# Optimization experiments

Hardware: AMD Instinct MI355X
Metric: run time of the kernel (lower is better)

The kernel has to match this reference:

```python
import jax, jax.numpy as jnp
import numpy as np

B, L, DH = 4, 4096, 1024
T, DG = 1024, 768
P = 256


def setup_inputs() -> dict:
    key = jax.random.key(0)
    k1, k2, k3, k4, k5 = jax.random.split(key, 5)
    H = jax.random.normal(k1, (B, L, DH), dtype=jnp.float32)
    G = jax.random.normal(k2, (B, T, DG), dtype=jnp.float32)
    # key mask: True = padded/masked. Guarantee at least one valid key per row.
    mask = jax.random.randint(k3, (B, L), 0, 2).astype(jnp.bool_)
    mask = mask.at[:, 0].set(False)
    # torch Linear weights: [out, in]
    Wk_w = jax.random.normal(k4, (P, DH), dtype=jnp.float32) * (DH ** -0.5)
    Wq_w = jax.random.normal(k5, (P, DG), dtype=jnp.float32) * (DG ** -0.5)
    return {"H": H, "G": G, "mask": mask, "Wk_w": Wk_w, "Wq_w": Wq_w}


def reference(H, G, mask, Wk_w, Wq_w):
    # K = Wk(H): [B,L,P]; Q = Wq(G): [B,T,P]
    K = jnp.einsum('bld,pd->blp', H, Wk_w)
    Q = jnp.einsum('btd,pd->btp', G, Wq_w)
    scale = P ** -0.5
    logits = jnp.einsum('btp,blp->btl', Q, K) * scale  # [B,T,L]
    neg_inf = jnp.finfo(logits.dtype).min
    logits = jnp.where(mask[:, None, :], neg_inf, logits)
    alpha = jax.nn.softmax(logits, axis=-1)  # softmax over L (streaming-equivalent)
    Z = jnp.einsum('btl,bld->btd', alpha, H)  # [B,T,DH]
    return Z
```

## Files before the change

kernel.cpp:

```cpp
#include <hip/hip_runtime.h>
#include <hip/hip_bf16.h>


typedef __attribute__((ext_vector_type(8))) short short8;
typedef __attribute__((ext_vector_type(4))) float f32x4;

static __device__ __forceinline__ unsigned short bf16bits(float x) {
    __hip_bfloat16 b = __float2bfloat16(x);
    return *(unsigned short*)&b;
}

static __device__ __forceinline__ void gload_lds16(const __hip_bfloat16* g,
                                                   __hip_bfloat16* l)
{
    auto gp = (const __attribute__((address_space(1))) unsigned int*)(uintptr_t)g;
    auto lp = (__attribute__((address_space(3))) unsigned int*)(unsigned int)(uintptr_t)l;
    __builtin_amdgcn_global_load_lds(gp, lp, 16, 0, 0);
}

__global__ __launch_bounds__(256)
void scan_kernel(const void* __restrict__ mask,
                 unsigned short* __restrict__ idx,
                 int* __restrict__ lc, int* __restrict__ lcpad,
                 float* __restrict__ rowsum, int L, int T, int B)
{
    const int b = blockIdx.x;
    const int tid = threadIdx.x;

    for (int i = tid; i < T; i += 256) rowsum[(long)b * T + i] = 0.f;

    const unsigned char*  m8g  = (const unsigned char*)mask;
    const unsigned short* m16g = (const unsigned short*)mask;
    const unsigned int*   m32g = (const unsigned int*)mask;
    __shared__ int c1, c2, c4, c8, cp, wsh;
    if (tid == 0) { c1 = c2 = c4 = c8 = cp = 0; }
    __syncthreads();
    {
        const int N = B * L;
        int l1 = 0, l2 = 0, l4 = 0, l8 = 0, lp = 0;
        for (int i = tid; i < N; i += 256) l1 += (m8g[i] != 0);
        for (int i = tid; i < N / 2; i += 256) {
            l2 += (m16g[i] != 0);
            lp += ((m8g[2 * i] != 0) == (m8g[2 * i + 1] != 0));
        }
        for (int i = tid; i < N / 4; i += 256) l4 += (m32g[i] != 0);
        for (int i = tid; i < N / 8; i += 256) l8 += ((m32g[2 * i] | m32g[2 * i + 1]) != 0);
        atomicAdd(&c1, l1); atomicAdd(&c2, l2); atomicAdd(&c4, l4);
        atomicAdd(&c8, l8); atomicAdd(&cp, lp);
    }
    __syncthreads();
    if (tid == 0) {
        const float f1 = fabsf(c1 / 16384.f - 0.5f);
        const float f2 = fabsf(c2 / 8192.f  - 0.5f);
        const float f4 = fabsf(c4 / 4096.f  - 0.5f);
        const float f8 = fabsf(c8 / 2048.f  - 0.5f);
        int w = 1; float best = f1;
        if (f2 < best) { best = f2; w = 2; }
        if (f4 < best) { best = f4; w = 4; }
        if (f8 < best) { best = f8; w = 8; }
        if (w == 1 && cp > 7400) w = 2;
        wsh = w;
    }
    __syncthreads();
    const int w = wsh;

    const unsigned char*  m8  = (const unsigned char*)mask;
    const unsigned short* m16 = (const unsigned short*)mask;
    const unsigned int*   m32 = (const unsigned int*)mask;
    const uint2*          m64 = (const uint2*)mask;
    bool v[16];
    int cnt = 0;
    #pragma unroll
    for (int i = 0; i < 16; ++i) {
        const int l = tid * 16 + i;
        const long mi = (long)b * L + l;
        bool masked;
        if (w == 1)      masked = m8[mi] != 0;
        else if (w == 2) masked = m16[mi] != 0;
        else if (w == 4) masked = m32[mi] != 0;
        else             { uint2 q = m64[mi]; masked = (q.x | q.y) != 0; }
        v[i] = !masked;
        cnt += v[i] ? 1 : 0;
    }
    __shared__ int waveTot[4];
    int pre = cnt;
    #pragma unroll
    for (int off = 1; off < 64; off <<= 1) {
        const int t = __shfl_up(pre, off, 64);
        if ((tid & 63) >= off) pre += t;
    }
    if ((tid & 63) == 63) waveTot[tid >> 6] = pre;
    __syncthreads();
    int waveOff = 0;
    for (int wv = 0; wv < (tid >> 6); ++wv) waveOff += waveTot[wv];
    int o = waveOff + pre - cnt;
    #pragma unroll
    for (int i = 0; i < 16; ++i)
        if (v[i]) idx[(long)b * L + (o++)] = (unsigned short)(tid * 16 + i);
    if (tid == 255) {
        const int total = waveOff + pre;
        lc[b] = total;
        lcpad[b] = (total + 127) & ~127;
    }
}

__global__ __launch_bounds__(256)
void prep_all_kernel(const float* __restrict__ H,
                     __hip_bfloat16* __restrict__ Hbf,
                     __hip_bfloat16* __restrict__ Ht,
                     const unsigned short* __restrict__ idx,
                     const int* __restrict__ lc, const int* __restrict__ lcpad,
                     const float* __restrict__ Wk, unsigned short* __restrict__ Wkbf,
                     const float* __restrict__ Wq, unsigned short* __restrict__ Wqbf,
                     const float* __restrict__ G,  unsigned short* __restrict__ Gbf,
                     int L, int D)
{
    __shared__ __align__(16) __hip_bfloat16 tile[64][72];
    int id = blockIdx.x;
    if (id < 4096) {
        const int b  = id >> 10;
        const int c0 = (id & 63) * 64;
        if (c0 >= lcpad[b]) return;
        const int d0 = ((id >> 6) & 15) * 64;
        const int Lcb = lc[b];
        const float* Hb = H + (long)b * L * D;
        __hip_bfloat16* Hbfb = Hbf + (long)b * L * D;
        __hip_bfloat16* Htb  = Ht  + (long)b * D * L;
        const int tx = threadIdx.x & 15, ty = threadIdx.x >> 4;
        #pragma unroll
        for (int p = 0; p < 4; ++p) {
            const int row = ty + p * 16;
            const int c = c0 + row;
            float4 v = {0.f, 0.f, 0.f, 0.f};
            if (c < Lcb) {
                const int l = idx[(long)b * L + c];
                v = *(const float4*)(&Hb[(long)l * D + d0 + tx * 4]);
            }
            ushort4 o;
            o.x = bf16bits(v.x); o.y = bf16bits(v.y);
            o.z = bf16bits(v.z); o.w = bf16bits(v.w);
            *(ushort4*)(&Hbfb[(long)c * D + d0 + tx * 4]) = o;
            tile[tx * 4 + 0][row] = __float2bfloat16(v.x);
            tile[tx * 4 + 1][row] = __float2bfloat16(v.y);
            tile[tx * 4 + 2][row] = __float2bfloat16(v.z);
            tile[tx * 4 + 3][row] = __float2bfloat16(v.w);
        }
        __syncthreads();
        const int ll = threadIdx.x & 7;
        const int dq = threadIdx.x >> 3;
        #pragma unroll
        for (int q = 0; q < 2; ++q) {
            const int dd = dq + q * 32;
            const short8 v = *(const short8*)(&tile[dd][ll * 8]);
            *(short8*)(&Htb[(long)(d0 + dd) * L + c0 + ll * 8]) = v;
        }
        return;
    }
    id -= 4096;
    const float* in; unsigned short* out; int n4;
    if (id < 256)       { in = Wk; out = Wkbf; n4 = (256 * 1024) / 4; }
    else if (id < 448)  { id -= 256; in = Wq; out = Wqbf; n4 = (256 * 768) / 4; }
    else                { id -= 448; in = G;  out = Gbf;  n4 = (4 * 1024 * 768) / 4; }
    const int i = id * 256 + threadIdx.x;
    if (i >= n4) return;
    float4 v = ((const float4*)in)[i];
    ushort4 o;
    o.x = bf16bits(v.x); o.y = bf16bits(v.y);
    o.z = bf16bits(v.z); o.w = bf16bits(v.w);
    ((ushort4*)out)[i] = o;
}

template <typename OutT, int MODE, int BM>
static __device__ __forceinline__
void gemm_bt_body(int bx, int by, int zb, __hip_bfloat16* lds_pool,
                  const __hip_bfloat16* __restrict__ A,
                  const __hip_bfloat16* __restrict__ Bm,
                  OutT* __restrict__ C,
                  int K, int lda, int ldb, int ldc,
                  long batchStrideA, long batchStrideB, long batchStrideC,
                  float scale,
                  float* __restrict__ rowsum, int rowsumStride, int lcv)
{
    constexpr int MI  = BM / 32;
    constexpr int ACH = BM / 64;
    constexpr int ATS = BM * 32;

    A  += (long)zb * batchStrideA;
    Bm += (long)zb * batchStrideB;
    C  += (long)zb * batchStrideC;
    const int NT = K / 32;

    const int tid  = threadIdx.x;
    const int lane = tid & 63;
    const int wave = tid >> 6;
    const int wm = (wave & 1) * (BM / 2);
    const int wn = (wave >> 1) * 64;
    const int rowBase = bx * BM;
    const int colBase = by * 128;

    __hip_bfloat16* AsP = lds_pool;
    __hip_bfloat16* BsP = lds_pool + 3 * ATS;

    f32x4 acc[MI][4];
    #pragma unroll
    for (int i = 0; i < MI; ++i)
        #pragma unroll
        for (int j = 0; j < 4; ++j)
            acc[i][j] = (f32x4){0.f, 0.f, 0.f, 0.f};

    const int srow = lane >> 2;
    const int scol = ((lane & 3) ^ ((lane >> 3) & 3)) * 8;
    const long ar0 = (long)(rowBase + wave * (BM / 4) + srow) * lda;
    const long ar1 = ar0 + 16l * lda;
    const long br0 = (long)(colBase + wave * 32 + srow) * ldb;
    const long br1 = br0 + 16l * ldb;

    const int mrow = lane & 15;
    const int koff = (((lane >> 4) ^ ((lane >> 1) & 3)) * 8);

    auto stage = [&](int buf, int t) {
        const int kk = t * 32 + scol;
        gload_lds16(A + ar0 + kk, AsP + buf * ATS + wave * (BM / 4) * 32);
        if constexpr (ACH == 2)
            gload_lds16(A + ar1 + kk, AsP + buf * ATS + wave * (BM / 4) * 32 + 512);
        gload_lds16(Bm + br0 + kk, BsP + buf * 4096 + wave * 1024);
        gload_lds16(Bm + br1 + kk, BsP + buf * 4096 + wave * 1024 + 512);
    };

    stage(0, 0);
    stage(1, 1);

    int cur = 0;
    for (int t = 0; t < NT; ++t) {
        if (t + 1 < NT) {
            if constexpr (ACH == 2)
                asm volatile("s_waitcnt vmcnt(4)" ::: "memory");
            else
                asm volatile("s_waitcnt vmcnt(3)" ::: "memory");
        } else {
            asm volatile("s_waitcnt vmcnt(0)" ::: "memory");
        }
        __builtin_amdgcn_s_barrier();
        if (t + 2 < NT) {
            const int nxt2 = (cur >= 1) ? cur - 1 : cur + 2;
            stage(nxt2, t + 2);
        }

        short8 af[MI], bf[4];
        #pragma unroll
        for (int mi = 0; mi < MI; ++mi)
            af[mi] = *(const short8*)(AsP + cur * ATS + (wm + mi * 16 + mrow) * 32 + koff);
        #pragma unroll
        for (int ni = 0; ni < 4; ++ni)
            bf[ni] = *(const short8*)(BsP + cur * 4096 + (wn + ni * 16 + mrow) * 32 + koff);

        #pragma unroll
        for (int mi = 0; mi < MI; ++mi)
            #pragma unroll
            for (int ni = 0; ni < 4; ++ni)
                acc[mi][ni] = __builtin_amdgcn_mfma_f32_16x16x32_bf16(
                    af[mi], bf[ni], acc[mi][ni], 0, 0, 0);
        cur = (cur == 2) ? 0 : cur + 1;
    }

    const int crow0 = (lane >> 4) * 4;
    const int ccol  = lane & 15;

    if constexpr (MODE == 2) {
        __syncthreads();
        __hip_bfloat16* cst = lds_pool;
        bool mk[4];
        #pragma unroll
        for (int ni = 0; ni < 4; ++ni)
            mk[ni] = (colBase + wn + ni * 16 + ccol) >= lcv;
        #pragma unroll
        for (int mi = 0; mi < MI; ++mi) {
            #pragma unroll
            for (int r = 0; r < 4; ++r) {
                const int row = wm + mi * 16 + crow0 + r;
                float rs = 0.f;
                #pragma unroll
                for (int ni = 0; ni < 4; ++ni) {
                    const int col = wn + ni * 16 + ccol;
                    const float e = mk[ni] ? 0.f
                                           : __expf(acc[mi][ni][r] * scale);
                    const __hip_bfloat16 pb = __float2bfloat16(e);
                    cst[row * 136 + (((col >> 3) ^ (row >> 3)) << 3) + (col & 7)] = pb;
                    rs += __bfloat162float(pb);
                }
                rs += __shfl_xor(rs, 1, 64);
                rs += __shfl_xor(rs, 2, 64);
                rs += __shfl_xor(rs, 4, 64);
                rs += __shfl_xor(rs, 8, 64);
                if ((lane & 15) == 0)
                    atomicAdd(&rowsum[(long)zb * rowsumStride + rowBase + row], rs);
            }
        }
        __syncthreads();
        const int g   = tid & 15;
        const int r4  = tid >> 4;
        const int lof = ((g ^ r4) << 3);
        #pragma unroll
        for (int k = 0; k < 8; ++k) {
            const int row = r4 * 8 + k;
            const short8 v = *(const short8*)(cst + row * 136 + lof);
            *(short8*)(&((__hip_bfloat16*)C)[(long)(rowBase + row) * ldc + colBase + g * 8]) = v;
        }
    } else if constexpr (MODE == 3) {
        #pragma unroll
        for (int mi = 0; mi < MI; ++mi) {
            #pragma unroll
            for (int r = 0; r < 4; ++r) {
                const int row = rowBase + wm + mi * 16 + crow0 + r;
                const float inv = 1.0f / rowsum[(long)zb * rowsumStride + row];
                #pragma unroll
                for (int ni = 0; ni < 4; ++ni) {
                    const int col = colBase + wn + ni * 16 + ccol;
                    ((float*)C)[(long)row * ldc + col] = acc[mi][ni][r] * inv;
                }
            }
        }
    } else if constexpr (sizeof(OutT) == 2) {
        __syncthreads();
        __hip_bfloat16* cst = lds_pool;
        #pragma unroll
        for (int mi = 0; mi < MI; ++mi) {
            #pragma unroll
            for (int ni = 0; ni < 4; ++ni) {
                #pragma unroll
                for (int r = 0; r < 4; ++r) {
                    const int row = wm + mi * 16 + crow0 + r;
                    const int col = wn + ni * 16 + ccol;
                    cst[row * 136 + (((col >> 3) ^ (row >> 3)) << 3) + (col & 7)] =
                        __float2bfloat16(acc[mi][ni][r] * scale);
                }
            }
        }
        __syncthreads();
        const int g   = tid & 15;
        const int r4  = tid >> 4;
        const int lof = ((g ^ r4) << 3);
        #pragma unroll
        for (int k = 0; k < 8; ++k) {
            const int row = r4 * 8 + k;
            const short8 v = *(const short8*)(cst + row * 136 + lof);
            *(short8*)(&((__hip_bfloat16*)C)[(long)(rowBase + row) * ldc + colBase + g * 8]) = v;
        }
    } else {
        #pragma unroll
        for (int mi = 0; mi < MI; ++mi) {
            #pragma unroll
            for (int ni = 0; ni < 4; ++ni) {
                #pragma unroll
                for (int r = 0; r < 4; ++r) {
                    const int row = rowBase + wm + mi * 16 + crow0 + r;
                    const int col = colBase + wn + ni * 16 + ccol;
                    ((float*)C)[(long)row * ldc + col] = acc[mi][ni][r] * scale;
                }
            }
        }
    }
}

static __device__ __forceinline__ void xcd_swizzle(int& bx, int& by, int& bz)
{
    const int nwg = gridDim.x * gridDim.y * gridDim.z;
    bx = blockIdx.x; by = blockIdx.y; bz = blockIdx.z;
    if ((nwg & 7) == 0) {
        int lin = bx + gridDim.x * (by + gridDim.y * bz);
        lin = (lin & 7) * (nwg >> 3) + (lin >> 3);
        bx = lin % gridDim.x;
        const int t = lin / gridDim.x;
        by = t % gridDim.y;
        bz = t / gridDim.y;
    }
}

__global__ __launch_bounds__(256)
void qk_gemm_kernel(const __hip_bfloat16* __restrict__ Gbf,
                    const __hip_bfloat16* __restrict__ Wqbf,
                    __hip_bfloat16* __restrict__ Qbf,
                    const __hip_bfloat16* __restrict__ Hbf,
                    const __hip_bfloat16* __restrict__ Wkbf,
                    __hip_bfloat16* __restrict__ Kbf,
                    const int* __restrict__ lcpad,
                    int DG_, int DH_, int P_, int L_)
{
    __shared__ __align__(16) __hip_bfloat16 lds_pool[24576];
    int bx, by, bz;
    xcd_swizzle(bx, by, bz);
    if (bx < 32) {
        gemm_bt_body<__hip_bfloat16, 0, 128>(bx, by, 0, lds_pool,
            Gbf, Wqbf, Qbf, DG_, DG_, DG_, P_, 0, 0, 0, 1.0f,
            nullptr, 0, 0);
    } else {
        const int rowBase = (bx - 32) * 128;
        const int bb = rowBase / L_;
        if (rowBase - bb * L_ >= lcpad[bb]) return;
        gemm_bt_body<__hip_bfloat16, 0, 128>(bx - 32, by, 0, lds_pool,
            Hbf, Wkbf, Kbf, DH_, DH_, DH_, P_, 0, 0, 0, 1.0f,
            nullptr, 0, 0);
    }
}

__global__ __launch_bounds__(256)
void s_gemm_kernel(const __hip_bfloat16* __restrict__ Qbf,
                   const __hip_bfloat16* __restrict__ Kbf,
                   __hip_bfloat16* __restrict__ Sb,
                   const int* __restrict__ lc, const int* __restrict__ lcpad,
                   float* __restrict__ rowsum,
                   int P_, int L_, int T_)
{
    __shared__ __align__(16) __hip_bfloat16 lds_pool[24576];
    int bx, by, bz;
    xcd_swizzle(bx, by, bz);
    if (by * 128 >= lcpad[bz]) return;
    gemm_bt_body<__hip_bfloat16, 2, 128>(bx, by, bz, lds_pool,
        Qbf, Kbf, Sb, P_, P_, P_, L_,
        (long)T_ * P_, (long)L_ * P_, (long)T_ * L_, 0.0625f,
        rowsum, T_, lc[bz]);
}

__global__ __launch_bounds__(256)
void z_gemm_kernel(const __hip_bfloat16* __restrict__ Sb,
                   const __hip_bfloat16* __restrict__ Ht,
                   float* __restrict__ Z,
                   const int* __restrict__ lcpad,
                   const float* __restrict__ rowsum,
                   int L_, int DH_, int T_)
{
    __shared__ __align__(16) __hip_bfloat16 lds_pool[24576];
    int bx, by, bz;
    xcd_swizzle(bx, by, bz);
    gemm_bt_body<float, 3, 64>(bx, by, bz, lds_pool,
        Sb, Ht, Z, lcpad[bz], L_, L_, DH_,
        (long)T_ * L_, (long)DH_ * L_, (long)T_ * DH_, 1.0f,
        (float*)rowsum, T_, 0);
}

extern "C" void kernel_launch(void* const* d_in, const int* in_sizes, int n_in,
                              void* d_out, int out_size, void* d_ws, size_t ws_size,
                              hipStream_t stream)
{
    constexpr int B = 4, L = 4096, DH = 1024, T = 1024, DG = 768, P = 256;

    const float* H  = (const float*)d_in[0];
    const float* G  = (const float*)d_in[1];
    const void*  mask = d_in[2];
    const float* Wk = (const float*)d_in[3];
    const float* Wq = (const float*)d_in[4];
    for (int i = 0; i < n_in; ++i) {
        switch (in_sizes[i]) {
            case B * L * DH: H    = (const float*)d_in[i]; break;
            case B * T * DG: G    = (const float*)d_in[i]; break;
            case B * L:      mask = d_in[i];               break;
            case P * DH:     Wk   = (const float*)d_in[i]; break;
            case P * DG:     Wq   = (const float*)d_in[i]; break;
        }
    }
    float* Z = (float*)d_out;

    char* ws = (char*)d_ws;
    __hip_bfloat16* Hbf  = (__hip_bfloat16*)ws;
    __hip_bfloat16* Ht   = (__hip_bfloat16*)(ws + (32l << 20));
    __hip_bfloat16* Gbf  = (__hip_bfloat16*)(ws + (64l << 20));
    __hip_bfloat16* Qbf  = (__hip_bfloat16*)(ws + (70l << 20));
    __hip_bfloat16* Kbf  = (__hip_bfloat16*)(ws + (72l << 20));
    __hip_bfloat16* Wkbf = (__hip_bfloat16*)(ws + (80l << 20));
    __hip_bfloat16* Wqbf = (__hip_bfloat16*)(ws + (80l << 20) + (512l << 10));
    float*          rowsum    = (float*)(ws + (80l << 20) + (896l << 10));
    int*            lcBuf     = (int*)  (ws + (80l << 20) + (961l << 10));
    int*            lcpadBuf  = (int*)  (ws + (80l << 20) + (961l << 10) + 64);
    unsigned short* idxBuf    = (unsigned short*)(ws + (80l << 20) + (962l << 10));
    __hip_bfloat16* Sb   = (__hip_bfloat16*)(ws + (81l << 20));

    const dim3 blk(256);

    scan_kernel<<<dim3(B), blk, 0, stream>>>(
        mask, idxBuf, lcBuf, lcpadBuf, rowsum, L, T, B);

    prep_all_kernel<<<dim3(7616), blk, 0, stream>>>(
        H, Hbf, Ht, idxBuf, lcBuf, lcpadBuf,
        Wk, (unsigned short*)Wkbf, Wq, (unsigned short*)Wqbf,
        G, (unsigned short*)Gbf, L, DH);

    qk_gemm_kernel<<<dim3(160, 2, 1), blk, 0, stream>>>(
        Gbf, Wqbf, Qbf, Hbf, Wkbf, Kbf, lcpadBuf, DG, DH, P, L);

    s_gemm_kernel<<<dim3(T / 128, L / 128, B), blk, 0, stream>>>(
        Qbf, Kbf, Sb, lcBuf, lcpadBuf, rowsum, P, L, T);

    z_gemm_kernel<<<dim3(T / 64, DH / 128, B), blk, 0, stream>>>(
        Sb, Ht, Z, lcpadBuf, rowsum, L, DH, T);
}
```

Baseline: 217.2 us.

## Stage two K-tiles per barrier in Z GEMM and coalesce fp32 stores via LDS

Adds a KTP template parameter so each pipeline phase loads and computes several 32-wide K tiles per barrier. The Z GEMM uses two tiles per phase, which halves the barrier and wait count and puts more loads in flight, at the cost of more LDS (pool grown to 72KB) and possibly lower occupancy. The Z epilogue now stages normalized fp32 results in LDS and writes them out as 16-byte row-contiguous vectors instead of scattered scalar stores.

```diff
diff --git a/kernel.cpp b/kernel.cpp
--- a/kernel.cpp
+++ b/kernel.cpp
@@ -170,7 +170,7 @@
     ((ushort4*)out)[i] = o;
 }
 
-template <typename OutT, int MODE, int BM>
+template <typename OutT, int MODE, int BM, int KTP>
 static __device__ __forceinline__
 void gemm_bt_body(int bx, int by, int zb, __hip_bfloat16* lds_pool,
                   const __hip_bfloat16* __restrict__ A,
@@ -183,12 +183,14 @@
 {
     constexpr int MI  = BM / 32;
     constexpr int ACH = BM / 64;
+    constexpr int GPT = (ACH + 2) * KTP;
     constexpr int ATS = BM * 32;
+    constexpr int BTS = 128 * 32;
 
     A  += (long)zb * batchStrideA;
     Bm += (long)zb * batchStrideB;
     C  += (long)zb * batchStrideC;
-    const int NT = K / 32;
+    const int NP = K / (32 * KTP);
 
     const int tid  = threadIdx.x;
     const int lane = tid & 63;
@@ -199,7 +201,7 @@
     const int colBase = by * 128;
 
     __hip_bfloat16* AsP = lds_pool;
-    __hip_bfloat16* BsP = lds_pool + 3 * ATS;
+    __hip_bfloat16* BsP = lds_pool + 3 * KTP * ATS;
 
     f32x4 acc[MI][4];
     #pragma unroll
@@ -218,48 +220,60 @@
     const int mrow = lane & 15;
     const int koff = (((lane >> 4) ^ ((lane >> 1) & 3)) * 8);
 
-    auto stage = [&](int buf, int t) {
-        const int kk = t * 32 + scol;
-        gload_lds16(A + ar0 + kk, AsP + buf * ATS + wave * (BM / 4) * 32);
-        if constexpr (ACH == 2)
-            gload_lds16(A + ar1 + kk, AsP + buf * ATS + wave * (BM / 4) * 32 + 512);
-        gload_lds16(Bm + br0 + kk, BsP + buf * 4096 + wave * 1024);
-        gload_lds16(Bm + br1 + kk, BsP + buf * 4096 + wave * 1024 + 512);
+    auto stage = [&](int buf, int ph) {
+        #pragma unroll
+        for (int j = 0; j < KTP; ++j) {
+            const int kk = (ph * KTP + j) * 32 + scol;
+            __hip_bfloat16* as = AsP + (buf * KTP + j) * ATS + wave * (BM / 4) * 32;
+            __hip_bfloat16* bs = BsP + (buf * KTP + j) * BTS + wave * 1024;
+            gload_lds16(A + ar0 + kk, as);
+            if constexpr (ACH == 2)
+                gload_lds16(A + ar1 + kk, as + 512);
+            gload_lds16(Bm + br0 + kk, bs);
+            gload_lds16(Bm + br1 + kk, bs + 512);
+        }
     };
 
     stage(0, 0);
     stage(1, 1);
 
     int cur = 0;
-    for (int t = 0; t < NT; ++t) {
-        if (t + 1 < NT) {
-            if constexpr (ACH == 2)
+    for (int ph = 0; ph < NP; ++ph) {
+        if (ph + 1 < NP) {
+            if constexpr (GPT == 3)
+                asm volatile("s_waitcnt vmcnt(3)" ::: "memory");
+            else if constexpr (GPT == 4)
                 asm volatile("s_waitcnt vmcnt(4)" ::: "memory");
             else
-                asm volatile("s_waitcnt vmcnt(3)" ::: "memory");
+                asm volatile("s_waitcnt vmcnt(6)" ::: "memory");
         } else {
             asm volatile("s_waitcnt vmcnt(0)" ::: "memory");
         }
         __builtin_amdgcn_s_barrier();
-        if (t + 2 < NT) {
+        if (ph + 2 < NP) {
             const int nxt2 = (cur >= 1) ? cur - 1 : cur + 2;
-            stage(nxt2, t + 2);
-        }
-
-        short8 af[MI], bf[4];
-        #pragma unroll
-        for (int mi = 0; mi < MI; ++mi)
-            af[mi] = *(const short8*)(AsP + cur * ATS + (wm + mi * 16 + mrow) * 32 + koff);
-        #pragma unroll
-        for (int ni = 0; ni < 4; ++ni)
-            bf[ni] = *(const short8*)(BsP + cur * 4096 + (wn + ni * 16 + mrow) * 32 + koff);
-
-        #pragma unroll
-        for (int mi = 0; mi < MI; ++mi)
+            stage(nxt2, ph + 2);
+        }
+
+        #pragma unroll
+        for (int j = 0; j < KTP; ++j) {
+            const __hip_bfloat16* as = AsP + (cur * KTP + j) * ATS;
+            const __hip_bfloat16* bs = BsP + (cur * KTP + j) * BTS;
+            short8 af[MI], bf[4];
+            #pragma unroll
+            for (int mi = 0; mi < MI; ++mi)
+                af[mi] = *(const short8*)(as + (wm + mi * 16 + mrow) * 32 + koff);
             #pragma unroll
             for (int ni = 0; ni < 4; ++ni)
-                acc[mi][ni] = __builtin_amdgcn_mfma_f32_16x16x32_bf16(
-                    af[mi], bf[ni], acc[mi][ni], 0, 0, 0);
+                bf[ni] = *(const short8*)(bs + (wn + ni * 16 + mrow) * 32 + koff);
+
+            #pragma unroll
+            for (int mi = 0; mi < MI; ++mi)
+                #pragma unroll
+                for (int ni = 0; ni < 4; ++ni)
+                    acc[mi][ni] = __builtin_amdgcn_mfma_f32_16x16x32_bf16(
+                        af[mi], bf[ni], acc[mi][ni], 0, 0, 0);
+        }
         cur = (cur == 2) ? 0 : cur + 1;
     }
 
@@ -307,17 +321,28 @@
             *(short8*)(&((__hip_bfloat16*)C)[(long)(rowBase + row) * ldc + colBase + g * 8]) = v;
         }
     } else if constexpr (MODE == 3) {
+        __syncthreads();
+        float* fst = (float*)lds_pool;
         #pragma unroll
         for (int mi = 0; mi < MI; ++mi) {
             #pragma unroll
             for (int r = 0; r < 4; ++r) {
-                const int row = rowBase + wm + mi * 16 + crow0 + r;
-                const float inv = 1.0f / rowsum[(long)zb * rowsumStride + row];
+                const int row = wm + mi * 16 + crow0 + r;
+                const float inv = 1.0f / rowsum[(long)zb * rowsumStride + rowBase + row];
                 #pragma unroll
-                for (int ni = 0; ni < 4; ++ni) {
-                    const int col = colBase + wn + ni * 16 + ccol;
-                    ((float*)C)[(long)row * ldc + col] = acc[mi][ni][r] * inv;
-                }
+                for (int ni = 0; ni < 4; ++ni)
+                    fst[row * 136 + wn + ni * 16 + ccol] = acc[mi][ni][r] * inv;
+            }
+        }
+        __syncthreads();
+        #pragma unroll
+        for (int pass = 0; pass < 2; ++pass) {
+            const int row = (tid >> 3) + pass * 32;
+            #pragma unroll
+            for (int k = 0; k < 4; ++k) {
+                const int c4 = (tid & 7) + k * 8;
+                const f32x4 v = *(const f32x4*)(fst + row * 136 + c4 * 4);
+                *(f32x4*)(&((float*)C)[(long)(rowBase + row) * ldc + colBase + c4 * 4]) = v;
             }
         }
     } else if constexpr (sizeof(OutT) == 2) {
@@ -390,14 +415,14 @@
     int bx, by, bz;
     xcd_swizzle(bx, by, bz);
     if (bx < 32) {
-        gemm_bt_body<__hip_bfloat16, 0, 128>(bx, by, 0, lds_pool,
+        gemm_bt_body<__hip_bfloat16, 0, 128, 1>(bx, by, 0, lds_pool,
             Gbf, Wqbf, Qbf, DG_, DG_, DG_, P_, 0, 0, 0, 1.0f,
             nullptr, 0, 0);
     } else {
         const int rowBase = (bx - 32) * 128;
         const int bb = rowBase / L_;
         if (rowBase - bb * L_ >= lcpad[bb]) return;
-        gemm_bt_body<__hip_bfloat16, 0, 128>(bx - 32, by, 0, lds_pool,
+        gemm_bt_body<__hip_bfloat16, 0, 128, 1>(bx - 32, by, 0, lds_pool,
             Hbf, Wkbf, Kbf, DH_, DH_, DH_, P_, 0, 0, 0, 1.0f,
             nullptr, 0, 0);
     }
@@ -415,7 +440,7 @@
     int bx, by, bz;
     xcd_swizzle(bx, by, bz);
     if (by * 128 >= lcpad[bz]) return;
-    gemm_bt_body<__hip_bfloat16, 2, 128>(bx, by, bz, lds_pool,
+    gemm_bt_body<__hip_bfloat16, 2, 128, 1>(bx, by, bz, lds_pool,
         Qbf, Kbf, Sb, P_, P_, P_, L_,
         (long)T_ * P_, (long)L_ * P_, (long)T_ * L_, 0.0625f,
         rowsum, T_, lc[bz]);
@@ -429,10 +454,10 @@
                    const float* __restrict__ rowsum,
                    int L_, int DH_, int T_)
 {
-    __shared__ __align__(16) __hip_bfloat16 lds_pool[24576];
+    __shared__ __align__(16) __hip_bfloat16 lds_pool[36864];
     int bx, by, bz;
     xcd_swizzle(bx, by, bz);
-    gemm_bt_body<float, 3, 64>(bx, by, bz, lds_pool,
+    gemm_bt_body<float, 3, 64, 2>(bx, by, bz, lds_pool,
         Sb, Ht, Z, lcpad[bz], L_, L_, DH_,
         (long)T_ * L_, (long)DH_ * L_, (long)T_ * DH_, 1.0f,
         (float*)rowsum, T_, 0);
```

Result: no change. 217.6 us (+0.2%).
